# Optimization experiments

Measured on AMD Instinct MI355X. Metric: run time of the kernel, lower is better.

The kernel has to match this reference:

```python
import jax, jax.numpy as jnp
import numpy as np

B, S = 128, 72
ITER = 16
D_MODEL, D_INPUT = 1024, 512
MEM = 25
HEADS, DH = 8, 64
N_SO, N_SA = 256, 64
NUM_CLASSES = 1968
MH = 16
VOCAB, TED = 32, 128
SA_SZ = N_SA * (N_SA + 1) // 2  # 2080
SO_SZ = N_SO * (N_SO + 1) // 2  # 32896
I_A, J_A = np.triu_indices(N_SA)
I_O, J_O = np.triu_indices(N_SO)


def _ln(x, g, b):
    m = x.mean(-1, keepdims=True)
    v = ((x - m) ** 2).mean(-1, keepdims=True)
    return (x - m) / jnp.sqrt(v + 1e-5) * g + b


def _glu(x):
    a, g = jnp.split(x, 2, axis=-1)
    return a * jax.nn.sigmoid(g)


def setup_inputs():
    key = jax.random.key(0)
    ks = iter(jax.random.split(key, 32))

    def u(shape, s):
        return jax.random.uniform(next(ks), shape, jnp.float32, -s, s)

    return {
        "x": jax.random.randint(next(ks), (B, S), 0, VOCAB),
        "emb": u((VOCAB, TED), 1.0),
        "kv_w": u((TED, D_INPUT), (1.0 / TED) ** 0.5),
        "kv_b": jnp.zeros((D_INPUT,), jnp.float32),
        "kv_ln_g": jnp.ones((D_INPUT,), jnp.float32),
        "kv_ln_b": jnp.zeros((D_INPUT,), jnp.float32),
        "q_w": u((SA_SZ, D_INPUT), (1.0 / SA_SZ) ** 0.5),
        "q_b": jnp.zeros((D_INPUT,), jnp.float32),
        "in_proj_w": u((D_INPUT, 3 * D_INPUT), (1.0 / D_INPUT) ** 0.5),
        "in_proj_b": jnp.zeros((3 * D_INPUT,), jnp.float32),
        "out_proj_w": u((D_INPUT, D_INPUT), (1.0 / D_INPUT) ** 0.5),
        "out_proj_b": jnp.zeros((D_INPUT,), jnp.float32),
        "syn_w": u((D_INPUT + D_MODEL, 2 * D_MODEL), (1.0 / (D_INPUT + D_MODEL)) ** 0.5),
        "syn_b": jnp.zeros((2 * D_MODEL,), jnp.float32),
        "syn_ln_g": jnp.ones((D_MODEL,), jnp.float32),
        "syn_ln_b": jnp.zeros((D_MODEL,), jnp.float32),
        "tp1_w": u((MEM, 2 * MH, D_MODEL), 1.0 / (MEM + 2 * MH) ** 0.5),
        "tp1_b": jnp.zeros((1, D_MODEL, 2 * MH), jnp.float32),
        "tp2_w": u((MH, 2, D_MODEL), 1.0 / (MH + 2) ** 0.5),
        "tp2_b": jnp.zeros((1, D_MODEL, 2), jnp.float32),
        "start_act": u((D_MODEL,), (1.0 / D_MODEL) ** 0.5),
        "start_trace": u((D_MODEL, MEM), (1.0 / (D_MODEL + MEM)) ** 0.5),
        "decay_action": jnp.zeros((SA_SZ,), jnp.float32),
        "decay_out": jnp.zeros((SO_SZ,), jnp.float32),
        "out_w": u((SO_SZ, NUM_CLASSES), (1.0 / SO_SZ) ** 0.5),
        "out_b": jnp.zeros((NUM_CLASSES,), jnp.float32),
    }


def _forward(x, emb, kv_w, kv_b, kv_ln_g, kv_ln_b, q_w, q_b, in_proj_w, in_proj_b,
             out_proj_w, out_proj_b, syn_w, syn_b, syn_ln_g, syn_ln_b,
             tp1_w, tp1_b, tp2_w, tp2_b, start_act, start_trace,
             decay_action, decay_out, out_w, out_b):
    Bn = x.shape[0]
    # kv features: embed -> linear -> layernorm  (B,S,D_INPUT)
    kv = _ln(emb[x] @ kv_w + kv_b, kv_ln_g, kv_ln_b)
    Wq, Wk, Wv = jnp.split(in_proj_w, 3, axis=1)
    bq, bk, bv = jnp.split(in_proj_b, 3, axis=0)
    K = (kv @ Wk + bk).reshape(Bn, -1, HEADS, DH)  # (B,S,H,Dh)
    V = (kv @ Wv + bv).reshape(Bn, -1, HEADS, DH)
    # decayed running-sync coefficients (decay params clamped to [0,15])
    r_a = jnp.exp(-jnp.clip(decay_action, 0.0, 15.0))
    r_o = jnp.exp(-jnp.clip(decay_out, 0.0, 15.0))
    act0 = jnp.broadcast_to(start_act, (Bn, D_MODEL))
    trace0 = jnp.broadcast_to(start_trace, (Bn, D_MODEL, MEM))
    so0 = act0[:, :N_SO]
    a_o0 = so0[:, I_O] * so0[:, J_O]           # initial out-sync alpha
    b_o0 = jnp.ones_like(a_o0)
    a_a0 = jnp.zeros((Bn, SA_SZ), kv.dtype)    # None-init == zeros under update rule
    b_a0 = jnp.zeros((Bn, SA_SZ), kv.dtype)

    def step(carry, _):
        act, trace, a_a, b_a, a_o, b_o = carry
        # action synchronisation (last N_SA neurons, triu outer product)
        sa = act[:, -N_SA:]
        a_a = r_a * a_a + sa[:, I_A] * sa[:, J_A]
        b_a = r_a * b_a + 1.0
        sync_a = a_a / jnp.sqrt(b_a)
        # single-query multihead attention over kv
        q = sync_a @ q_w + q_b
        qh = (q @ Wq + bq).reshape(Bn, HEADS, DH)
        scores = jnp.einsum('bhd,bshd->bhs', qh, K) / (DH ** 0.5)
        attn = jax.nn.softmax(scores, axis=-1)
        o = jnp.einsum('bhs,bshd->bhd', attn, V).reshape(Bn, D_INPUT)
        o = o @ out_proj_w + out_proj_b
        # synapses: concat -> linear -> GLU -> layernorm
        pre = jnp.concatenate([o, act], axis=-1)
        state = _ln(_glu(pre @ syn_w + syn_b), syn_ln_g, syn_ln_b)
        # shift trace, append new state
        trace = jnp.concatenate([trace[:, :, 1:], state[:, :, None]], axis=-1)
        # per-neuron NLM: SuperLinear -> GLU -> SuperLinear -> GLU -> squeeze
        h = _glu(jnp.einsum('bdm,mhd->bdh', trace, tp1_w) + tp1_b)      # (B,D,MH)
        act = _glu(jnp.einsum('bdm,mhd->bdh', h, tp2_w) + tp2_b)[..., 0]  # (B,D)
        # out synchronisation (first N_SO neurons)
        so = act[:, :N_SO]
        a_o = r_o * a_o + so[:, I_O] * so[:, J_O]
        b_o = r_o * b_o + 1.0
        sync_o = a_o / jnp.sqrt(b_o)
        pred = sync_o @ out_w + out_b                                   # (B,C)
        lp = jax.nn.log_softmax(pred, axis=-1)
        ne = -jnp.sum(jnp.exp(lp) * lp, axis=-1) / jnp.log(jnp.float32(NUM_CLASSES))
        cert = jnp.stack([ne, 1.0 - ne], axis=-1)                       # (B,2)
        return (act, trace, a_a, b_a, a_o, b_o), (pred, cert)

    _, (preds, certs) = jax.lax.scan(step, (act0, trace0, a_a0, b_a0, a_o0, b_o0), None, length=ITER)
    predictions = jnp.moveaxis(preds, 0, -1)   # (B,C,ITER)
    certainties = jnp.moveaxis(certs, 0, -1)   # (B,2,ITER)
    return predictions, certainties


def reference(x, emb, kv_w, kv_b, kv_ln_g, kv_ln_b, q_w, q_b, in_proj_w, in_proj_b,
              out_proj_w, out_proj_b, syn_w, syn_b, syn_ln_g, syn_ln_b,
              tp1_w, tp1_b, tp2_w, tp2_b, start_act, start_trace,
              decay_action, decay_out, out_w, out_b):
    return _forward(x, emb, kv_w, kv_b, kv_ln_g, kv_ln_b, q_w, q_b, in_proj_w, in_proj_b,
                    out_proj_w, out_proj_b, syn_w, syn_b, syn_ln_g, syn_ln_b,
                    tp1_w, tp1_b, tp2_w, tp2_b, start_act, start_trace,
                    decay_action, decay_out, out_w, out_b)
```

## Files before the change

kernel.cpp:

```cpp
#include <hip/hip_runtime.h>
#include <math.h>

#define BB 128
#define SS 72
#define NITER 16
#define D_IN 512
#define D_MODEL 1024
#define MEMN 25
#define HEADS 8
#define DHH 64
#define N_SO 256
#define N_SA 64
#define SA_SZ 2080
#define SO_SZ 32896
#define NCLS 1968
#define TED 128
#define VOCAB 32
#define ROWS (BB*SS)
#define TRACE_SLOTS (MEMN + NITER)

#define BGN 64
#define BGKS 16
#define BGKLEN 2056
#define BGSTEPS 33
#define NPART 1984
#define WHLD 1984
#define WCHUNKS 124
#define SYNZ 6

typedef _Float16 half_t;
typedef _Float16 half8 __attribute__((ext_vector_type(8)));
typedef float f32x4v __attribute__((ext_vector_type(4)));

__device__ __forceinline__ float sigmoidf_(float x){ return 1.f/(1.f+expf(-x)); }

__device__ __forceinline__ float bsum256(float v, float* red){
  int tid = threadIdx.x; red[tid] = v; __syncthreads();
#pragma unroll
  for (int s = 128; s > 0; s >>= 1){ if (tid < s) red[tid] += red[tid+s]; __syncthreads(); }
  float r = red[0]; __syncthreads(); return r;
}

__device__ __forceinline__ long triu_off(int n, int i){
  return (long)i*n - ((long)i*(i-1))/2;
}

__device__ __forceinline__ int swzA(int b){ return b ^ (((b>>9)&1)<<5); }

__global__ void k_conv(const float* __restrict__ src, half_t* __restrict__ dst, int n){
  int gid = blockIdx.x*256 + threadIdx.x;
  if (gid < n) dst[gid] = (half_t)src[gid];
}

__global__ void k_convslice(const float* __restrict__ src, int ldsrc, int col0,
                            half_t* __restrict__ dst, int rows, int cols){
  int gid = blockIdx.x*256 + threadIdx.x;
  if (gid >= rows*cols) return;
  int r = gid / cols, c = gid % cols;
  dst[gid] = (half_t)src[(size_t)r*ldsrc + col0 + c];
}

__global__ void k_embed_h(const int* __restrict__ x, const half_t* __restrict__ embh,
                          half_t* __restrict__ out){
  int gid = blockIdx.x*256 + threadIdx.x;
  if (gid >= ROWS*(TED/8)) return;
  int row = gid >> 4, c0 = (gid & 15)*8;
  *(half8*)(out + (size_t)row*TED + c0) = *(const half8*)(embh + (size_t)x[row]*TED + c0);
}

__global__ void k_init_pairs(int n, int npairs, const float* __restrict__ decay,
                             int2* __restrict__ pairs, float* __restrict__ rv){
  int p = blockIdx.x*256 + threadIdx.x;
  if (p >= npairs) return;
  double nn = (double)n;
  double disc = (2.0*nn+1.0)*(2.0*nn+1.0) - 8.0*(double)p;
  int i = (int)floor(((2.0*nn+1.0) - sqrt(disc))*0.5);
  if (i < 0) i = 0; if (i > n-1) i = n-1;
  while (i+1 < n && triu_off(n, i+1) <= (long)p) i++;
  while (i > 0 && triu_off(n, i) > (long)p) i--;
  int j = i + (int)((long)p - triu_off(n, i));
  pairs[p] = make_int2(i, j);
  float dc = decay[p]; dc = fminf(fmaxf(dc, 0.f), 15.f);
  rv[p] = expf(-dc);
}

__global__ void k_init_act(const float* __restrict__ sa, float* __restrict__ act){
  int gid = blockIdx.x*256 + threadIdx.x;
  if (gid >= BB*D_MODEL) return;
  act[gid] = sa[gid & 1023];
}

__global__ void k_zero(float* __restrict__ p, int n){
  int gid = blockIdx.x*256 + threadIdx.x;
  if (gid < n) p[gid] = 0.f;
}

__global__ void k_init_trace(const float* __restrict__ st, float* __restrict__ trace){
  int gid = blockIdx.x*256 + threadIdx.x;
  if (gid >= BB*MEMN*D_MODEL) return;
  int d = gid & 1023;
  int m = (gid >> 10) % MEMN;
  int b = (gid >> 10) / MEMN;
  trace[(size_t)b*TRACE_SLOTS*D_MODEL + (size_t)m*D_MODEL + d] = st[d*MEMN + m];
}

__global__ void k_init_ao(const float* __restrict__ sa, const int2* __restrict__ pairs,
                          float* __restrict__ ao){
  int p = blockIdx.x*256 + threadIdx.x;
  if (p >= SO_SZ) return;
  int b = blockIdx.y;
  int2 ij = pairs[p];
  ao[(size_t)b*SO_SZ + p] = sa[ij.x]*sa[ij.y];
}

__global__ void k_convw(const float* __restrict__ W, half_t* __restrict__ Wh){
  int gid = blockIdx.x*256 + threadIdx.x;
  if (gid >= SO_SZ*WCHUNKS) return;
  int row = gid / WCHUNKS, ch = gid - row*WCHUNKS;
  int c0 = ch*16;
  half_t* dst = Wh + (size_t)row*WHLD + c0;
  if (ch < 123){
    const float4* src = (const float4*)(W + (size_t)row*NCLS + c0);
    float4 f0 = src[0], f1 = src[1], f2 = src[2], f3 = src[3];
    half8 h0, h1;
    h0[0]=(half_t)f0.x; h0[1]=(half_t)f0.y; h0[2]=(half_t)f0.z; h0[3]=(half_t)f0.w;
    h0[4]=(half_t)f1.x; h0[5]=(half_t)f1.y; h0[6]=(half_t)f1.z; h0[7]=(half_t)f1.w;
    h1[0]=(half_t)f2.x; h1[1]=(half_t)f2.y; h1[2]=(half_t)f2.z; h1[3]=(half_t)f2.w;
    h1[4]=(half_t)f3.x; h1[5]=(half_t)f3.y; h1[6]=(half_t)f3.z; h1[7]=(half_t)f3.w;
    *(half8*)dst = h0; *(half8*)(dst+8) = h1;
  } else {
    half8 zz;
#pragma unroll
    for (int j = 0; j < 8; j++) zz[j] = (half_t)0.f;
    *(half8*)dst = zz; *(half8*)(dst+8) = zz;
  }
}

__global__ void k_colsum(const float* __restrict__ vec, const float* __restrict__ W,
                         int ldw, const float* __restrict__ addb,
                         float* __restrict__ out, int N, int K){
  int col = blockIdx.x*256 + threadIdx.x;
  if (col >= N) return;
  float s = addb ? addb[col] : 0.f;
  for (int k = 0; k < K; k++) s = fmaf(vec[k], W[(size_t)k*ldw + col], s);
  out[col] = s;
}

template<int MB>
__global__ void k_gemm(const float* __restrict__ A, int lda,
                       const float* __restrict__ W, int ldw, int wrow0, int wcol0,
                       const float* __restrict__ bias,
                       float* __restrict__ C, int ldc, int N, int K){
  constexpr int KC = 32;
  const int tid = threadIdx.x;
  const int col = blockIdx.x*256 + tid;
  const int row0 = blockIdx.y*MB;
  __shared__ float As[MB][KC];
  float acc[MB];
#pragma unroll
  for (int r = 0; r < MB; r++) acc[r] = 0.f;
  for (int kk = 0; kk < K; kk += KC){
    __syncthreads();
    for (int idx = tid; idx < MB*KC; idx += 256){
      int r = idx / KC, k = idx % KC;
      As[r][k] = A[(size_t)(row0+r)*lda + kk + k];
    }
    __syncthreads();
#pragma unroll
    for (int k = 0; k < KC; k++){
      float w = W[(size_t)(wrow0+kk+k)*ldw + wcol0 + col];
#pragma unroll
      for (int r = 0; r < MB; r++) acc[r] = fmaf(As[r][k], w, acc[r]);
    }
  }
#pragma unroll
  for (int r = 0; r < MB; r++){
    size_t o = (size_t)(row0+r)*ldc + col;
    C[o] = acc[r] + (bias ? bias[col] : 0.f);
  }
}

__global__ __launch_bounds__(256)
void k_pgemm(const half_t* __restrict__ Ah, int ldah,
             const half_t* __restrict__ Wh16, const float* __restrict__ bias,
             float* __restrict__ C, int ksteps){
  __shared__ half_t As[2][128*64];
  __shared__ half_t Ws[2][64*66];
  const int tid = threadIdx.x;
  const int nb0 = blockIdx.x * 64;
  const int row0 = blockIdx.y * 128;
  const int l = tid & 63, wv = tid >> 6;
  const int mw = (wv >> 1) * 64, nw = (wv & 1) * 32;
  const int c = l & 15, g = l >> 4;

  f32x4v acc[4][2];
#pragma unroll
  for (int i = 0; i < 4; i++)
#pragma unroll
    for (int j2 = 0; j2 < 2; j2++)
#pragma unroll
      for (int r = 0; r < 4; r++) acc[i][j2][r] = 0.f;

  auto stage = [&](int s, int buf){
#pragma unroll
    for (int it = 0; it < 4; it++){
      int ch = tid + it*256;
      int m = ch >> 3, kl = (ch & 7)*8;
      half8 v = *(const half8*)(Ah + (size_t)(row0+m)*ldah + s*64 + kl);
      *(half8*)((char*)(&As[buf][0]) + swzA(ch*16)) = v;
    }
    {
      int k = tid >> 2, cs = (tid & 3) * 16;
      const half_t* wr = Wh16 + (size_t)(s*64 + k) * D_IN + nb0 + cs;
      char* dst = (char*)(&Ws[buf][0]) + (size_t)(k*66 + cs) * 2;
      union { half8 v; unsigned int u[4]; } p0, p1;
      p0.v = *(const half8*)wr; p1.v = *(const half8*)(wr + 8);
#pragma unroll
      for (int q = 0; q < 4; q++){
        ((unsigned int*)dst)[q]        = p0.u[q];
        ((unsigned int*)(dst + 16))[q] = p1.u[q];
      }
    }
  };

  stage(0, 0);
  __syncthreads();
  for (int s = 0; s < ksteps; s++){
    int buf = s & 1;
    if (s + 1 < ksteps) stage(s+1, buf^1);
#pragma unroll
    for (int h = 0; h < 2; h++){
      half8 a8[4];
#pragma unroll
      for (int mb = 0; mb < 4; mb++)
        a8[mb] = *(const half8*)((const char*)(&As[buf][0]) +
                   swzA(((mw + mb*16 + c)*64 + h*32 + g*8)*2));
#pragma unroll
      for (int nb = 0; nb < 2; nb++){
        half8 b8;
        const half_t* wp = &Ws[buf][(h*32 + g*8)*66 + nw + nb*16 + c];
#pragma unroll
        for (int j = 0; j < 8; j++) b8[j] = wp[j*66];
#pragma unroll
        for (int mb = 0; mb < 4; mb++)
          acc[mb][nb] = __builtin_amdgcn_mfma_f32_16x16x32_f16(a8[mb], b8, acc[mb][nb], 0, 0, 0);
      }
    }
    __syncthreads();
  }
#pragma unroll
  for (int mb = 0; mb < 4; mb++)
#pragma unroll
    for (int nb = 0; nb < 2; nb++){
      int m = mw + mb*16 + g*4;
      int n = nb0 + nw + nb*16 + c;
      float bv = bias[n];
#pragma unroll
      for (int r = 0; r < 4; r++)
        C[(size_t)(row0 + m + r) * D_IN + n] = acc[mb][nb][r] + bv;
    }
}

__global__ __launch_bounds__(256)
void k_syn16(const half_t* __restrict__ Ah, const half_t* __restrict__ Wh16,
             float* __restrict__ outp){
  __shared__ half_t As[2][128*64];
  __shared__ half_t Ws[2][64*66];
  const int tid = threadIdx.x;
  const int nb0 = blockIdx.x * 64;
  const int z = blockIdx.y;
  const int l = tid & 63, wv = tid >> 6;
  const int mw = (wv >> 1) * 64, nw = (wv & 1) * 32;
  const int c = l & 15, g = l >> 4;
  const int kbase = z * 256;

  f32x4v acc[4][2];
#pragma unroll
  for (int i = 0; i < 4; i++)
#pragma unroll
    for (int j2 = 0; j2 < 2; j2++)
#pragma unroll
      for (int r = 0; r < 4; r++) acc[i][j2][r] = 0.f;

  auto stage = [&](int s, int buf){
#pragma unroll
    for (int it = 0; it < 4; it++){
      int ch = tid + it*256;
      int m = ch >> 3, kl = (ch & 7)*8;
      half8 v = *(const half8*)(Ah + (size_t)m*1536 + kbase + s*64 + kl);
      *(half8*)((char*)(&As[buf][0]) + swzA(ch*16)) = v;
    }
    {
      int k = tid >> 2, cs = (tid & 3) * 16;
      const half_t* wr = Wh16 + (size_t)(kbase + s*64 + k) * 2048 + nb0 + cs;
      char* dst = (char*)(&Ws[buf][0]) + (size_t)(k*66 + cs) * 2;
      union { half8 v; unsigned int u[4]; } p0, p1;
      p0.v = *(const half8*)wr; p1.v = *(const half8*)(wr + 8);
#pragma unroll
      for (int q = 0; q < 4; q++){
        ((unsigned int*)dst)[q]        = p0.u[q];
        ((unsigned int*)(dst + 16))[q] = p1.u[q];
      }
    }
  };

  stage(0, 0);
  __syncthreads();
  for (int s = 0; s < 4; s++){
    int buf = s & 1;
    if (s + 1 < 4) stage(s+1, buf^1);
#pragma unroll
    for (int h = 0; h < 2; h++){
      half8 a8[4];
#pragma unroll
      for (int mb = 0; mb < 4; mb++)
        a8[mb] = *(const half8*)((const char*)(&As[buf][0]) +
                   swzA(((mw + mb*16 + c)*64 + h*32 + g*8)*2));
#pragma unroll
      for (int nb = 0; nb < 2; nb++){
        half8 b8;
        const half_t* wp = &Ws[buf][(h*32 + g*8)*66 + nw + nb*16 + c];
#pragma unroll
        for (int j = 0; j < 8; j++) b8[j] = wp[j*66];
#pragma unroll
        for (int mb = 0; mb < 4; mb++)
          acc[mb][nb] = __builtin_amdgcn_mfma_f32_16x16x32_f16(a8[mb], b8, acc[mb][nb], 0, 0, 0);
      }
    }
    __syncthreads();
  }
  float* pz = outp + (size_t)z * BB * 2048;
#pragma unroll
  for (int mb = 0; mb < 4; mb++)
#pragma unroll
    for (int nb = 0; nb < 2; nb++){
      int m = mw + mb*16 + g*4;
      int n = nb0 + nw + nb*16 + c;
#pragma unroll
      for (int r = 0; r < 4; r++)
        pz[(size_t)(m + r) * 2048 + n] = acc[mb][nb][r];
    }
}

__global__ void k_cat16(const float* __restrict__ obuf, const float* __restrict__ act,
                        half_t* __restrict__ Ah){
  int gid = blockIdx.x*256 + threadIdx.x;
  if (gid >= BB*192) return;
  int row = gid / 192, c = (gid - row*192)*8;
  const float* src = (c < D_IN) ? (obuf + (size_t)row*D_IN + c)
                                : (act + (size_t)row*D_MODEL + (c - D_IN));
  float4 f0 = *(const float4*)src, f1 = *(const float4*)(src + 4);
  half8 h;
  h[0]=(half_t)f0.x; h[1]=(half_t)f0.y; h[2]=(half_t)f0.z; h[3]=(half_t)f0.w;
  h[4]=(half_t)f1.x; h[5]=(half_t)f1.y; h[6]=(half_t)f1.z; h[7]=(half_t)f1.w;
  *(half8*)(Ah + (size_t)row*1536 + c) = h;
}

__global__ void k_gemmq(const float* __restrict__ A, const float* __restrict__ W,
                        float* __restrict__ qpart){
  constexpr int KC = 32;
  const int tid = threadIdx.x;
  const int col = blockIdx.x*256 + tid;
  const int row0 = blockIdx.y*4;
  const int z = blockIdx.z;
  const int kstart = z*544;
  const int kend = min(SA_SZ, kstart + 544);
  __shared__ float As[4][KC];
  float acc[4] = {0.f,0.f,0.f,0.f};
  for (int kk = kstart; kk < kend; kk += KC){
    __syncthreads();
    for (int idx = tid; idx < 4*KC; idx += 256){
      int r = idx / KC, k = idx % KC;
      As[r][k] = A[(size_t)(row0+r)*SA_SZ + kk + k];
    }
    __syncthreads();
#pragma unroll
    for (int k = 0; k < KC; k++){
      float w = W[(size_t)(kk+k)*D_IN + col];
#pragma unroll
      for (int r = 0; r < 4; r++) acc[r] = fmaf(As[r][k], w, acc[r]);
    }
  }
#pragma unroll
  for (int r = 0; r < 4; r++)
    qpart[(size_t)z*BB*D_IN + (size_t)(row0+r)*D_IN + col] = acc[r];
}

__global__ void k_gemm2srcZ(const float* __restrict__ A1, const float* __restrict__ A2,
                            const float* __restrict__ W1, const float* __restrict__ W2,
                            float* __restrict__ outp){
  constexpr int MB = 8, KC = 32;
  const int tid = threadIdx.x;
  const int col = blockIdx.x*256 + tid;
  const int row0 = blockIdx.y*MB;
  const int z = blockIdx.z;
  __shared__ float As[MB][KC];
  float acc[MB];
#pragma unroll
  for (int r = 0; r < MB; r++) acc[r] = 0.f;
  for (int kk = z*256; kk < z*256 + 256; kk += KC){
    __syncthreads();
    for (int idx = tid; idx < MB*KC; idx += 256){
      int r = idx / KC, k = idx % KC;
      int kg = kk + k;
      As[r][k] = (kg < D_IN) ? A1[(size_t)(row0+r)*D_IN + kg]
                             : A2[(size_t)(row0+r)*D_MODEL + kg - D_IN];
    }
    __syncthreads();
    const float* Wp = (kk < D_IN) ? W1 : W2;
#pragma unroll
    for (int k = 0; k < KC; k++){
      float w = Wp[(size_t)(kk+k)*2048 + col];
#pragma unroll
      for (int r = 0; r < MB; r++) acc[r] = fmaf(As[r][k], w, acc[r]);
    }
  }
#pragma unroll
  for (int r = 0; r < MB; r++)
    outp[(size_t)z*BB*2048 + (size_t)(row0+r)*2048 + col] = acc[r];
}

__global__ void k_ln_h(const float* __restrict__ X, const float* __restrict__ g,
                       const float* __restrict__ bta, half_t* __restrict__ Y, int D){
  const int row = blockIdx.x, tid = threadIdx.x;
  __shared__ float red[256];
  const float* xr = X + (size_t)row*D;
  float s = 0.f;
  for (int c = tid; c < D; c += 256) s += xr[c];
  float mean = bsum256(s, red) / (float)D;
  float s2 = 0.f;
  for (int c = tid; c < D; c += 256){ float d = xr[c]-mean; s2 += d*d; }
  float var = bsum256(s2, red) / (float)D;
  float inv = 1.f / sqrtf(var + 1e-5f);
  half_t* yr = Y + (size_t)row*D;
  for (int c = tid; c < D; c += 256) yr[c] = (half_t)((xr[c]-mean)*inv*g[c] + bta[c]);
}

__global__ void k_glu_ln(const float* __restrict__ synpart, const float* __restrict__ bias2,
                         const float* __restrict__ g, const float* __restrict__ bta,
                         float* __restrict__ traceSlot){
  const int b = blockIdx.x, tid = threadIdx.x;
  __shared__ float vals[D_MODEL];
  __shared__ float red[256];
  for (int c = tid; c < 1024; c += 256){
    float a = bias2[c], gg = bias2[c+1024];
#pragma unroll
    for (int z = 0; z < SYNZ; z++){
      const float* sp = synpart + (size_t)z*BB*2048 + (size_t)b*2048;
      a  += sp[c];
      gg += sp[c+1024];
    }
    vals[c] = a * sigmoidf_(gg);
  }
  __syncthreads();
  float s = 0.f;
  for (int c = tid; c < 1024; c += 256) s += vals[c];
  float mean = bsum256(s, red) * (1.f/1024.f);
  float s2 = 0.f;
  for (int c = tid; c < 1024; c += 256){ float d = vals[c]-mean; s2 += d*d; }
  float var = bsum256(s2, red) * (1.f/1024.f);
  float inv = 1.f / sqrtf(var + 1e-5f);
  float* out = traceSlot + (size_t)b*(TRACE_SLOTS*D_MODEL);
  for (int c = tid; c < 1024; c += 256) out[c] = (vals[c]-mean)*inv*g[c] + bta[c];
}

__global__ void k_attn(const float* __restrict__ qpart, const float* __restrict__ bqf,
                       const float* __restrict__ Km, const float* __restrict__ Vm,
                       float* __restrict__ o){
  const int bh = blockIdx.x, b = bh >> 3, h = bh & 7;
  const int tid = threadIdx.x;
  __shared__ float qs[DHH];
  __shared__ float attn[SS];
  __shared__ float red[128];
  if (tid < DHH){
    int d = h*DHH + tid;
    float qv = bqf[d];
#pragma unroll
    for (int z = 0; z < 4; z++) qv += qpart[(size_t)z*BB*D_IN + (size_t)b*D_IN + d];
    qs[tid] = qv;
  }
  __syncthreads();
  float sc = -1e30f;
  if (tid < SS){
    const float* kp = Km + ((size_t)(b*SS+tid)*HEADS + h)*DHH;
    float d = 0.f;
#pragma unroll
    for (int i = 0; i < DHH; i++) d = fmaf(qs[i], kp[i], d);
    sc = d * 0.125f;
  }
  red[tid] = sc; __syncthreads();
  for (int s2 = 64; s2 > 0; s2 >>= 1){ if (tid < s2) red[tid] = fmaxf(red[tid], red[tid+s2]); __syncthreads(); }
  float m = red[0]; __syncthreads();
  float e = (tid < SS) ? expf(sc - m) : 0.f;
  red[tid] = e; __syncthreads();
  for (int s2 = 64; s2 > 0; s2 >>= 1){ if (tid < s2) red[tid] += red[tid+s2]; __syncthreads(); }
  float inv = 1.f / red[0]; __syncthreads();
  if (tid < SS) attn[tid] = e * inv;
  __syncthreads();
  if (tid < DHH){
    const float* vp = Vm + ((size_t)(b*SS)*HEADS + h)*DHH + tid;
    float acc = 0.f;
    for (int s2 = 0; s2 < SS; s2++) acc = fmaf(attn[s2], vp[(size_t)s2*D_IN], acc);
    o[(size_t)b*D_IN + h*DHH + tid] = acc;
  }
}

__global__ void k_neuron(const float* __restrict__ trace,
                         const float* __restrict__ tp1w, const float* __restrict__ tp1b,
                         const float* __restrict__ tp2w, const float* __restrict__ tp2b,
                         float* __restrict__ act, int t){
  int gid = blockIdx.x*256 + threadIdx.x;
  if (gid >= BB*D_MODEL) return;
  int b = gid >> 10, d = gid & 1023;
  const float* tr = trace + (size_t)b*(TRACE_SLOTS*D_MODEL) + (size_t)(t+1)*D_MODEL + d;
  float trv[MEMN];
#pragma unroll
  for (int m = 0; m < MEMN; m++) trv[m] = tr[(size_t)m*D_MODEL];
  float o0 = tp2b[d*2+0], o1 = tp2b[d*2+1];
#pragma unroll
  for (int j = 0; j < 16; j++){
    const float* wpj = tp1w + (size_t)j*1024 + d;
    const float* wpg = tp1w + (size_t)(j+16)*1024 + d;
    float hj = tp1b[d*32 + j];
    float hg = tp1b[d*32 + j + 16];
#pragma unroll
    for (int m = 0; m < MEMN; m++){
      float tv = trv[m];
      hj = fmaf(tv, wpj[(size_t)m*32*1024], hj);
      hg = fmaf(tv, wpg[(size_t)m*32*1024], hg);
    }
    float hgv = hj * sigmoidf_(hg);
    o0 = fmaf(hgv, tp2w[(size_t)(j*2+0)*1024 + d], o0);
    o1 = fmaf(hgv, tp2w[(size_t)(j*2+1)*1024 + d], o1);
  }
  act[gid] = o0 * sigmoidf_(o1);
}

__global__ void k_syncA(const float* __restrict__ act, const float* __restrict__ rv,
                        const int2* __restrict__ pairs, float* __restrict__ aa,
                        float* __restrict__ syncv, int t){
  int p = blockIdx.x*256 + threadIdx.x;
  if (p >= SA_SZ) return;
  int b = blockIdx.y;
  int2 ij = pairs[p];
  const float* ab = act + (size_t)b*D_MODEL + (D_MODEL - N_SA);
  float r = rv[p];
  size_t idx = (size_t)b*SA_SZ + p;
  float a = fmaf(r, aa[idx], ab[ij.x]*ab[ij.y]);
  aa[idx] = a;
  float bb = 0.f;
  for (int i = 0; i <= t; i++) bb = fmaf(r, bb, 1.f);
  syncv[idx] = a / sqrtf(bb);
}

__global__ void k_syncO(const float* __restrict__ act, const float* __restrict__ rv,
                        const int2* __restrict__ pairs, float* __restrict__ ao,
                        half_t* __restrict__ syncv, int t){
  int p = blockIdx.x*256 + threadIdx.x;
  if (p >= SO_SZ) return;
  int b = blockIdx.y;
  int2 ij = pairs[p];
  const float* ab = act + (size_t)b*D_MODEL;
  float r = rv[p];
  size_t idx = (size_t)b*SO_SZ + p;
  float a = fmaf(r, ao[idx], ab[ij.x]*ab[ij.y]);
  ao[idx] = a;
  float bb = 1.f;
  for (int i = 0; i <= t; i++) bb = fmaf(r, bb, 1.f);
  syncv[idx] = (half_t)(a / sqrtf(bb));
}

__global__ __launch_bounds__(256)
void k_bigemm2h(const half_t* __restrict__ Ah, const half_t* __restrict__ Wh,
                float* __restrict__ part){
  __shared__ half_t As[2][128*64];
  __shared__ half_t Ws[2][64*66];
  const int tid = threadIdx.x;
  const int z = blockIdx.y;
  const int nb0 = blockIdx.x * BGN;
  const int l = tid & 63, wv = tid >> 6;
  const int mw = (wv >> 1) * 64, nw = (wv & 1) * 32;
  const int c = l & 15, g = l >> 4;
  const int k0 = z * BGKLEN;

  f32x4v acc[4][2];
#pragma unroll
  for (int i = 0; i < 4; i++)
#pragma unroll
    for (int j2 = 0; j2 < 2; j2++)
#pragma unroll
      for (int r = 0; r < 4; r++) acc[i][j2][r] = 0.f;

  auto stage = [&](int s, int buf){
    const int kv = min(64, BGKLEN - s*64);
#pragma unroll
    for (int it = 0; it < 4; it++){
      int ch = tid + it*256;
      int m = ch >> 3, kg = ch & 7, kl = kg*8;
      half8 v;
      if (kl < kv) v = *(const half8*)(Ah + (size_t)m*SO_SZ + k0 + s*64 + kl);
      else {
#pragma unroll
        for (int j = 0; j < 8; j++) v[j] = (half_t)0.f;
      }
      *(half8*)((char*)(&As[buf][0]) + swzA(ch*16)) = v;
    }
    {
      int k = tid >> 2, cs = (tid & 3) * 16;
      const half_t* wr = Wh + (size_t)(k0 + s*64 + k) * WHLD + nb0 + cs;
      char* dst = (char*)(&Ws[buf][0]) + (size_t)(k*66 + cs) * 2;
      union { half8 v; unsigned int u[4]; } p0, p1;
      if (k < kv){ p0.v = *(const half8*)wr; p1.v = *(const half8*)(wr + 8); }
      else {
#pragma unroll
        for (int j = 0; j < 8; j++){ p0.v[j] = (half_t)0.f; p1.v[j] = (half_t)0.f; }
      }
#pragma unroll
      for (int q = 0; q < 4; q++){
        ((unsigned int*)dst)[q]        = p0.u[q];
        ((unsigned int*)(dst + 16))[q] = p1.u[q];
      }
    }
  };

  stage(0, 0);
  __syncthreads();
  for (int s = 0; s < BGSTEPS; s++){
    int buf = s & 1;
    if (s + 1 < BGSTEPS) stage(s+1, buf^1);
#pragma unroll
    for (int h = 0; h < 2; h++){
      half8 a8[4];
#pragma unroll
      for (int mb = 0; mb < 4; mb++)
        a8[mb] = *(const half8*)((const char*)(&As[buf][0]) +
                   swzA(((mw + mb*16 + c)*64 + h*32 + g*8)*2));
#pragma unroll
      for (int nb = 0; nb < 2; nb++){
        half8 b8;
        const half_t* wp = &Ws[buf][(h*32 + g*8)*66 + nw + nb*16 + c];
#pragma unroll
        for (int j = 0; j < 8; j++) b8[j] = wp[j*66];
#pragma unroll
        for (int mb = 0; mb < 4; mb++)
          acc[mb][nb] = __builtin_amdgcn_mfma_f32_16x16x32_f16(a8[mb], b8, acc[mb][nb], 0, 0, 0);
      }
    }
    __syncthreads();
  }
  float* pz = part + (size_t)z * 128 * NPART;
#pragma unroll
  for (int mb = 0; mb < 4; mb++)
#pragma unroll
    for (int nb = 0; nb < 2; nb++){
      int m = mw + mb*16 + g*4;
      int n = nb0 + nw + nb*16 + c;
#pragma unroll
      for (int r = 0; r < 4; r++)
        pz[(size_t)(m + r) * NPART + n] = acc[mb][nb][r];
    }
}

__global__ void k_output(const float* __restrict__ part, const float* __restrict__ outb,
                         float* __restrict__ dout, int t){
  const int b = blockIdx.x, tid = threadIdx.x;
  __shared__ float pred[NCLS];
  __shared__ float red[256];
  float lmax = -1e30f;
  for (int c = tid; c < NCLS; c += 256){
    float s = outb[c];
    const float* pp = part + (size_t)b*NPART + c;
#pragma unroll
    for (int z = 0; z < BGKS; z++) s += pp[(size_t)z*128*NPART];
    pred[c] = s;
    dout[((size_t)b*NCLS + c)*NITER + t] = s;
    lmax = fmaxf(lmax, s);
  }
  red[tid] = lmax; __syncthreads();
  for (int s2 = 128; s2 > 0; s2 >>= 1){ if (tid < s2) red[tid] = fmaxf(red[tid], red[tid+s2]); __syncthreads(); }
  float m = red[0]; __syncthreads();
  float se = 0.f;
  for (int c = tid; c < NCLS; c += 256) se += expf(pred[c]-m);
  float Z = bsum256(se, red);
  float logZ = m + logf(Z);
  float ent = 0.f;
  for (int c = tid; c < NCLS; c += 256){ float lp = pred[c]-logZ; ent += expf(lp)*lp; }
  float E = bsum256(ent, red);
  if (tid == 0){
    float ne = -E * (1.f/logf((float)NCLS));
    float* cp = dout + (size_t)BB*NCLS*NITER + (size_t)b*2*NITER + t;
    cp[0]     = ne;
    cp[NITER] = 1.f - ne;
  }
}

extern "C" void kernel_launch(void* const* d_in, const int* in_sizes, int n_in,
                              void* d_out, int out_size, void* d_ws, size_t ws_size,
                              hipStream_t stream){
  const int*   x           = (const int*)  d_in[0];
  const float* emb         = (const float*)d_in[1];
  const float* kv_w        = (const float*)d_in[2];
  const float* kv_b        = (const float*)d_in[3];
  const float* kv_ln_g     = (const float*)d_in[4];
  const float* kv_ln_b     = (const float*)d_in[5];
  const float* q_w         = (const float*)d_in[6];
  const float* q_b         = (const float*)d_in[7];
  const float* in_proj_w   = (const float*)d_in[8];
  const float* in_proj_b   = (const float*)d_in[9];
  const float* out_proj_w  = (const float*)d_in[10];
  const float* out_proj_b  = (const float*)d_in[11];
  const float* syn_w       = (const float*)d_in[12];
  const float* syn_b       = (const float*)d_in[13];
  const float* syn_ln_g    = (const float*)d_in[14];
  const float* syn_ln_b    = (const float*)d_in[15];
  const float* tp1_w       = (const float*)d_in[16];
  const float* tp1_b       = (const float*)d_in[17];
  const float* tp2_w       = (const float*)d_in[18];
  const float* tp2_b       = (const float*)d_in[19];
  const float* start_act   = (const float*)d_in[20];
  const float* start_trace = (const float*)d_in[21];
  const float* decay_action= (const float*)d_in[22];
  const float* decay_out   = (const float*)d_in[23];
  const float* out_w       = (const float*)d_in[24];
  const float* out_b       = (const float*)d_in[25];
  float* dout = (float*)d_out;

  float* w = (float*)d_ws;
  size_t off = 0;
  auto alloc = [&](size_t n){ n = (n + 3) & ~(size_t)3; float* p = w + off; off += n; return p; };
  float* region0 = alloc((size_t)BGKS*128*NPART);
  float* region1 = alloc((size_t)ROWS*D_IN);
  float* Kmat    = alloc((size_t)ROWS*D_IN);
  float* Vmat    = alloc((size_t)ROWS*D_IN);
  float* trace   = alloc((size_t)BB*TRACE_SLOTS*D_MODEL);
  half_t* sync_oh= (half_t*)alloc((size_t)BB*SO_SZ/2);
  float* a_a     = alloc((size_t)BB*SA_SZ);
  float* sync_a  = alloc((size_t)BB*SA_SZ);
  float* act     = alloc((size_t)BB*D_MODEL);
  float* qpart   = alloc((size_t)4*BB*D_IN);
  float* obuf    = alloc((size_t)BB*D_IN);
  float* qfw     = alloc((size_t)SA_SZ*D_IN);
  float* Wf2     = alloc((size_t)D_IN*2048);
  float* bqf     = alloc(D_IN);
  float* bias2   = alloc(2048);
  float* r_a     = alloc(SA_SZ);
  float* r_o     = alloc(SO_SZ);
  int2*  pairsA  = (int2*)alloc(2*SA_SZ);
  int2*  pairsO  = (int2*)alloc(2*SO_SZ);
  half_t* embh   = (half_t*)alloc((size_t)VOCAB*TED/2);
  half_t* kvwh   = (half_t*)alloc((size_t)TED*D_IN/2);
  half_t* Wkh    = (half_t*)alloc((size_t)D_IN*D_IN/2);
  half_t* Wvh    = (half_t*)alloc((size_t)D_IN*D_IN/2);
  half_t* Wh     = (half_t*)alloc(((size_t)SO_SZ*WHLD)/2);
  half_t* Ah16   = (half_t*)alloc((size_t)BB*1536/2);
  half_t* Wsynh  = (half_t*)alloc((size_t)1536*2048/2);
  const bool use_syn16 = (off * sizeof(float) <= ws_size);

  half_t* embx_h = (half_t*)region0;
  half_t* kvh    = (half_t*)region0;
  float* part    = region0;
  float* synpart = region0;
  float* kvbuf = region1;
  float* a_o   = region1;

  dim3 blk(256);

  k_conv<<<(VOCAB*TED+255)/256, blk, 0, stream>>>(emb, embh, VOCAB*TED);
  k_convslice<<<(TED*D_IN+255)/256, blk, 0, stream>>>(kv_w, D_IN, 0, kvwh, TED, D_IN);
  k_convslice<<<(D_IN*D_IN+255)/256, blk, 0, stream>>>(in_proj_w, 1536, 512,  Wkh, D_IN, D_IN);
  k_convslice<<<(D_IN*D_IN+255)/256, blk, 0, stream>>>(in_proj_w, 1536, 1024, Wvh, D_IN, D_IN);
  k_embed_h<<<(ROWS*(TED/8)+255)/256, blk, 0, stream>>>(x, embh, embx_h);
  k_pgemm<<<dim3(8, ROWS/128), blk, 0, stream>>>(embx_h, TED, kvwh, kv_b, kvbuf, TED/64);
  k_ln_h<<<ROWS, blk, 0, stream>>>(kvbuf, kv_ln_g, kv_ln_b, kvh, D_IN);
  k_pgemm<<<dim3(8, ROWS/128), blk, 0, stream>>>(kvh, D_IN, Wkh, in_proj_b+512,  Kmat, D_IN/64);
  k_pgemm<<<dim3(8, ROWS/128), blk, 0, stream>>>(kvh, D_IN, Wvh, in_proj_b+1024, Vmat, D_IN/64);
  k_gemm<4><<<dim3(2, SA_SZ/4), blk, 0, stream>>>(q_w, D_IN, in_proj_w, 1536, 0, 0, nullptr, qfw, D_IN, D_IN, D_IN);
  k_gemm<4><<<dim3(8, D_IN/4), blk, 0, stream>>>(out_proj_w, D_IN, syn_w, 2048, 0, 0, nullptr, Wf2, 2048, 2048, D_IN);
  k_colsum<<<2, blk, 0, stream>>>(q_b, in_proj_w, 1536, in_proj_b, bqf, D_IN, D_IN);
  k_colsum<<<8, blk, 0, stream>>>(out_proj_b, syn_w, 2048, syn_b, bias2, 2048, D_IN);
  k_convw<<<(SO_SZ*WCHUNKS+255)/256, blk, 0, stream>>>(out_w, Wh);
  if (use_syn16){
    k_conv<<<(512*2048+255)/256, blk, 0, stream>>>(Wf2, Wsynh, 512*2048);
    k_conv<<<(1024*2048+255)/256, blk, 0, stream>>>(syn_w + (size_t)512*2048, Wsynh + (size_t)512*2048, 1024*2048);
  }
  k_init_pairs<<<(SA_SZ+255)/256, blk, 0, stream>>>(N_SA, SA_SZ, decay_action, pairsA, r_a);
  k_init_pairs<<<(SO_SZ+255)/256, blk, 0, stream>>>(N_SO, SO_SZ, decay_out,    pairsO, r_o);
  k_init_act<<<(BB*D_MODEL+255)/256, blk, 0, stream>>>(start_act, act);
  k_zero<<<(BB*SA_SZ+255)/256, blk, 0, stream>>>(a_a, BB*SA_SZ);
  k_init_trace<<<(BB*MEMN*D_MODEL+255)/256, blk, 0, stream>>>(start_trace, trace);
  k_init_ao<<<dim3((SO_SZ+255)/256, BB), blk, 0, stream>>>(start_act, pairsO, a_o);

  for (int t = 0; t < NITER; t++){
    k_syncA<<<dim3((SA_SZ+255)/256, BB), blk, 0, stream>>>(act, r_a, pairsA, a_a, sync_a, t);
    k_gemmq<<<dim3(2, 32, 4), blk, 0, stream>>>(sync_a, qfw, qpart);
    k_attn<<<BB*HEADS, 128, 0, stream>>>(qpart, bqf, Kmat, Vmat, obuf);
    if (use_syn16){
      k_cat16<<<(BB*192+255)/256, blk, 0, stream>>>(obuf, act, Ah16);
      k_syn16<<<dim3(32, SYNZ), blk, 0, stream>>>(Ah16, Wsynh, synpart);
    } else {
      k_gemm2srcZ<<<dim3(8, 16, SYNZ), blk, 0, stream>>>(obuf, act, Wf2, syn_w, synpart);
    }
    k_glu_ln<<<BB, blk, 0, stream>>>(synpart, bias2, syn_ln_g, syn_ln_b, trace + (size_t)(MEMN+t)*D_MODEL);
    k_neuron<<<(BB*D_MODEL+255)/256, blk, 0, stream>>>(trace, tp1_w, tp1_b, tp2_w, tp2_b, act, t);
    k_syncO<<<dim3((SO_SZ+255)/256, BB), blk, 0, stream>>>(act, r_o, pairsO, a_o, sync_oh, t);
    k_bigemm2h<<<dim3(31, BGKS), blk, 0, stream>>>(sync_oh, Wh, part);
    k_output<<<BB, blk, 0, stream>>>(part, out_b, dout, t);
  }
}
```

Baseline: 3.041 ms.

## Fuse syncA into gemmq, drop cat16, store q weights in half, merge setup conversions

The action-synchronisation update is computed inside the q GEMM's A-tile load, using ping-pong buffers for the decay state so the separate syncA kernel and the sync_a buffer go away. The fp16 concat input for the synapse GEMM is written directly by k_attn, k_neuron and k_init_act, which removes k_cat16. The fused q weight matrix is converted to fp16 to halve its reads. Several setup conversion kernels are merged into fewer launches. Each gemmq block now recomputes the sync values, including the per-element decay loop, and the half-precision q weights add rounding error.

```diff
diff --git a/kernel.cpp b/kernel.cpp
--- a/kernel.cpp
+++ b/kernel.cpp
@@ -52,12 +52,28 @@
   if (gid < n) dst[gid] = (half_t)src[gid];
 }
 
-__global__ void k_convslice(const float* __restrict__ src, int ldsrc, int col0,
-                            half_t* __restrict__ dst, int rows, int cols){
+#define CV0 (VOCAB*TED)
+#define CV1 (CV0 + TED*D_IN)
+#define CV2 (CV1 + D_IN*D_IN)
+#define CV3 (CV2 + D_IN*D_IN)
+__global__ void k_convall(const float* __restrict__ emb, const float* __restrict__ kv_w,
+                          const float* __restrict__ in_proj_w,
+                          half_t* __restrict__ embh, half_t* __restrict__ kvwh,
+                          half_t* __restrict__ Wkh, half_t* __restrict__ Wvh){
   int gid = blockIdx.x*256 + threadIdx.x;
-  if (gid >= rows*cols) return;
-  int r = gid / cols, c = gid % cols;
-  dst[gid] = (half_t)src[(size_t)r*ldsrc + col0 + c];
+  if (gid < CV0){ embh[gid] = (half_t)emb[gid]; return; }
+  if (gid < CV1){ int i = gid - CV0; kvwh[i] = (half_t)kv_w[i]; return; }
+  if (gid < CV2){ int i = gid - CV1; int r = i >> 9, c = i & 511;
+                  Wkh[i] = (half_t)in_proj_w[(size_t)r*1536 + 512 + c]; return; }
+  if (gid < CV3){ int i = gid - CV2; int r = i >> 9, c = i & 511;
+                  Wvh[i] = (half_t)in_proj_w[(size_t)r*1536 + 1024 + c]; return; }
+}
+
+__global__ void k_convsyn(const float* __restrict__ Wf2, const float* __restrict__ syn_w,
+                          half_t* __restrict__ Wsynh){
+  int gid = blockIdx.x*256 + threadIdx.x;
+  if (gid >= 1536*2048) return;
+  Wsynh[gid] = (half_t)((gid < 512*2048) ? Wf2[gid] : syn_w[gid]);
 }
 
 __global__ void k_embed_h(const int* __restrict__ x, const half_t* __restrict__ embh,
@@ -84,10 +100,14 @@
   rv[p] = expf(-dc);
 }
 
-__global__ void k_init_act(const float* __restrict__ sa, float* __restrict__ act){
+__global__ void k_init_act(const float* __restrict__ sa, float* __restrict__ act,
+                           half_t* __restrict__ Ah16){
   int gid = blockIdx.x*256 + threadIdx.x;
   if (gid >= BB*D_MODEL) return;
-  act[gid] = sa[gid & 1023];
+  int b = gid >> 10, d = gid & 1023;
+  float v = sa[d];
+  act[gid] = v;
+  Ah16[(size_t)b*1536 + 512 + d] = (half_t)v;
 }
 
 __global__ void k_zero(float* __restrict__ p, int n){
@@ -342,22 +362,10 @@
     }
 }
 
-__global__ void k_cat16(const float* __restrict__ obuf, const float* __restrict__ act,
-                        half_t* __restrict__ Ah){
-  int gid = blockIdx.x*256 + threadIdx.x;
-  if (gid >= BB*192) return;
-  int row = gid / 192, c = (gid - row*192)*8;
-  const float* src = (c < D_IN) ? (obuf + (size_t)row*D_IN + c)
-                                : (act + (size_t)row*D_MODEL + (c - D_IN));
-  float4 f0 = *(const float4*)src, f1 = *(const float4*)(src + 4);
-  half8 h;
-  h[0]=(half_t)f0.x; h[1]=(half_t)f0.y; h[2]=(half_t)f0.z; h[3]=(half_t)f0.w;
-  h[4]=(half_t)f1.x; h[5]=(half_t)f1.y; h[6]=(half_t)f1.z; h[7]=(half_t)f1.w;
-  *(half8*)(Ah + (size_t)row*1536 + c) = h;
-}
-
-__global__ void k_gemmq(const float* __restrict__ A, const float* __restrict__ W,
-                        float* __restrict__ qpart){
+__global__ void k_gemmq(const float* __restrict__ act,
+                        const float* __restrict__ r_a, const int2* __restrict__ pairsA,
+                        const float* __restrict__ aaIn, float* __restrict__ aaOut,
+                        const half_t* __restrict__ Wh, float* __restrict__ qpart, int t){
   constexpr int KC = 32;
   const int tid = threadIdx.x;
   const int col = blockIdx.x*256 + tid;
@@ -365,18 +373,29 @@
   const int z = blockIdx.z;
   const int kstart = z*544;
   const int kend = min(SA_SZ, kstart + 544);
+  const bool writer = (blockIdx.x == 0);
   __shared__ float As[4][KC];
   float acc[4] = {0.f,0.f,0.f,0.f};
   for (int kk = kstart; kk < kend; kk += KC){
     __syncthreads();
-    for (int idx = tid; idx < 4*KC; idx += 256){
-      int r = idx / KC, k = idx % KC;
-      As[r][k] = A[(size_t)(row0+r)*SA_SZ + kk + k];
+    if (tid < 4*KC){
+      int r = tid >> 5, k = tid & 31;
+      int p = kk + k;
+      int b = row0 + r;
+      int2 ij = pairsA[p];
+      const float* ab = act + (size_t)b*D_MODEL + (D_MODEL - N_SA);
+      float rv = r_a[p];
+      size_t idx = (size_t)b*SA_SZ + p;
+      float a = fmaf(rv, aaIn[idx], ab[ij.x]*ab[ij.y]);
+      if (writer) aaOut[idx] = a;
+      float bb = 0.f;
+      for (int i = 0; i <= t; i++) bb = fmaf(rv, bb, 1.f);
+      As[r][k] = a / sqrtf(bb);
     }
     __syncthreads();
 #pragma unroll
     for (int k = 0; k < KC; k++){
-      float w = W[(size_t)(kk+k)*D_IN + col];
+      float w = (float)Wh[(size_t)(kk+k)*D_IN + col];
 #pragma unroll
       for (int r = 0; r < 4; r++) acc[r] = fmaf(As[r][k], w, acc[r]);
     }
@@ -466,7 +485,7 @@
 
 __global__ void k_attn(const float* __restrict__ qpart, const float* __restrict__ bqf,
                        const float* __restrict__ Km, const float* __restrict__ Vm,
-                       float* __restrict__ o){
+                       float* __restrict__ o, half_t* __restrict__ Ah16){
   const int bh = blockIdx.x, b = bh >> 3, h = bh & 7;
   const int tid = threadIdx.x;
   __shared__ float qs[DHH];
@@ -501,14 +520,16 @@
     const float* vp = Vm + ((size_t)(b*SS)*HEADS + h)*DHH + tid;
     float acc = 0.f;
     for (int s2 = 0; s2 < SS; s2++) acc = fmaf(attn[s2], vp[(size_t)s2*D_IN], acc);
-    o[(size_t)b*D_IN + h*DHH + tid] = acc;
+    int d = h*DHH + tid;
+    o[(size_t)b*D_IN + d] = acc;
+    Ah16[(size_t)b*1536 + d] = (half_t)acc;
   }
 }
 
 __global__ void k_neuron(const float* __restrict__ trace,
                          const float* __restrict__ tp1w, const float* __restrict__ tp1b,
                          const float* __restrict__ tp2w, const float* __restrict__ tp2b,
-                         float* __restrict__ act, int t){
+                         float* __restrict__ act, half_t* __restrict__ Ah16, int t){
   int gid = blockIdx.x*256 + threadIdx.x;
   if (gid >= BB*D_MODEL) return;
   int b = gid >> 10, d = gid & 1023;
@@ -533,24 +554,9 @@
     o0 = fmaf(hgv, tp2w[(size_t)(j*2+0)*1024 + d], o0);
     o1 = fmaf(hgv, tp2w[(size_t)(j*2+1)*1024 + d], o1);
   }
-  act[gid] = o0 * sigmoidf_(o1);
-}
-
-__global__ void k_syncA(const float* __restrict__ act, const float* __restrict__ rv,
-                        const int2* __restrict__ pairs, float* __restrict__ aa,
-                        float* __restrict__ syncv, int t){
-  int p = blockIdx.x*256 + threadIdx.x;
-  if (p >= SA_SZ) return;
-  int b = blockIdx.y;
-  int2 ij = pairs[p];
-  const float* ab = act + (size_t)b*D_MODEL + (D_MODEL - N_SA);
-  float r = rv[p];
-  size_t idx = (size_t)b*SA_SZ + p;
-  float a = fmaf(r, aa[idx], ab[ij.x]*ab[ij.y]);
-  aa[idx] = a;
-  float bb = 0.f;
-  for (int i = 0; i <= t; i++) bb = fmaf(r, bb, 1.f);
-  syncv[idx] = a / sqrtf(bb);
+  float v = o0 * sigmoidf_(o1);
+  act[gid] = v;
+  Ah16[(size_t)b*1536 + 512 + d] = (half_t)v;
 }
 
 __global__ void k_syncO(const float* __restrict__ act, const float* __restrict__ rv,
@@ -734,8 +740,7 @@
   float* Vmat    = alloc((size_t)ROWS*D_IN);
   float* trace   = alloc((size_t)BB*TRACE_SLOTS*D_MODEL);
   half_t* sync_oh= (half_t*)alloc((size_t)BB*SO_SZ/2);
-  float* a_a     = alloc((size_t)BB*SA_SZ);
-  float* sync_a  = alloc((size_t)BB*SA_SZ);
+  float* a_aP    = alloc((size_t)2*BB*SA_SZ);
   float* act     = alloc((size_t)BB*D_MODEL);
   float* qpart   = alloc((size_t)4*BB*D_IN);
   float* obuf    = alloc((size_t)BB*D_IN);
@@ -751,6 +756,7 @@
   half_t* kvwh   = (half_t*)alloc((size_t)TED*D_IN/2);
   half_t* Wkh    = (half_t*)alloc((size_t)D_IN*D_IN/2);
   half_t* Wvh    = (half_t*)alloc((size_t)D_IN*D_IN/2);
+  half_t* qfwh   = (half_t*)alloc((size_t)SA_SZ*D_IN/2);
   half_t* Wh     = (half_t*)alloc(((size_t)SO_SZ*WHLD)/2);
   half_t* Ah16   = (half_t*)alloc((size_t)BB*1536/2);
   half_t* Wsynh  = (half_t*)alloc((size_t)1536*2048/2);
@@ -765,10 +771,7 @@
 
   dim3 blk(256);
 
-  k_conv<<<(VOCAB*TED+255)/256, blk, 0, stream>>>(emb, embh, VOCAB*TED);
-  k_convslice<<<(TED*D_IN+255)/256, blk, 0, stream>>>(kv_w, D_IN, 0, kvwh, TED, D_IN);
-  k_convslice<<<(D_IN*D_IN+255)/256, blk, 0, stream>>>(in_proj_w, 1536, 512,  Wkh, D_IN, D_IN);
-  k_convslice<<<(D_IN*D_IN+255)/256, blk, 0, stream>>>(in_proj_w, 1536, 1024, Wvh, D_IN, D_IN);
+  k_convall<<<(CV3+255)/256, blk, 0, stream>>>(emb, kv_w, in_proj_w, embh, kvwh, Wkh, Wvh);
   k_embed_h<<<(ROWS*(TED/8)+255)/256, blk, 0, stream>>>(x, embh, embx_h);
   k_pgemm<<<dim3(8, ROWS/128), blk, 0, stream>>>(embx_h, TED, kvwh, kv_b, kvbuf, TED/64);
   k_ln_h<<<ROWS, blk, 0, stream>>>(kvbuf, kv_ln_g, kv_ln_b, kvh, D_IN);
@@ -776,32 +779,30 @@
   k_pgemm<<<dim3(8, ROWS/128), blk, 0, stream>>>(kvh, D_IN, Wvh, in_proj_b+1024, Vmat, D_IN/64);
   k_gemm<4><<<dim3(2, SA_SZ/4), blk, 0, stream>>>(q_w, D_IN, in_proj_w, 1536, 0, 0, nullptr, qfw, D_IN, D_IN, D_IN);
   k_gemm<4><<<dim3(8, D_IN/4), blk, 0, stream>>>(out_proj_w, D_IN, syn_w, 2048, 0, 0, nullptr, Wf2, 2048, 2048, D_IN);
+  k_conv<<<(SA_SZ*D_IN+255)/256, blk, 0, stream>>>(qfw, qfwh, SA_SZ*D_IN);
   k_colsum<<<2, blk, 0, stream>>>(q_b, in_proj_w, 1536, in_proj_b, bqf, D_IN, D_IN);
   k_colsum<<<8, blk, 0, stream>>>(out_proj_b, syn_w, 2048, syn_b, bias2, 2048, D_IN);
   k_convw<<<(SO_SZ*WCHUNKS+255)/256, blk, 0, stream>>>(out_w, Wh);
-  if (use_syn16){
-    k_conv<<<(512*2048+255)/256, blk, 0, stream>>>(Wf2, Wsynh, 512*2048);
-    k_conv<<<(1024*2048+255)/256, blk, 0, stream>>>(syn_w + (size_t)512*2048, Wsynh + (size_t)512*2048, 1024*2048);
-  }
+  if (use_syn16)
+    k_convsyn<<<(1536*2048+255)/256, blk, 0, stream>>>(Wf2, syn_w, Wsynh);
   k_init_pairs<<<(SA_SZ+255)/256, blk, 0, stream>>>(N_SA, SA_SZ, decay_action, pairsA, r_a);
   k_init_pairs<<<(SO_SZ+255)/256, blk, 0, stream>>>(N_SO, SO_SZ, decay_out,    pairsO, r_o);
-  k_init_act<<<(BB*D_MODEL+255)/256, blk, 0, stream>>>(start_act, act);
-  k_zero<<<(BB*SA_SZ+255)/256, blk, 0, stream>>>(a_a, BB*SA_SZ);
+  k_init_act<<<(BB*D_MODEL+255)/256, blk, 0, stream>>>(start_act, act, Ah16);
+  k_zero<<<(2*BB*SA_SZ+255)/256, blk, 0, stream>>>(a_aP, 2*BB*SA_SZ);
   k_init_trace<<<(BB*MEMN*D_MODEL+255)/256, blk, 0, stream>>>(start_trace, trace);
   k_init_ao<<<dim3((SO_SZ+255)/256, BB), blk, 0, stream>>>(start_act, pairsO, a_o);
 
   for (int t = 0; t < NITER; t++){
-    k_syncA<<<dim3((SA_SZ+255)/256, BB), blk, 0, stream>>>(act, r_a, pairsA, a_a, sync_a, t);
-    k_gemmq<<<dim3(2, 32, 4), blk, 0, stream>>>(sync_a, qfw, qpart);
-    k_attn<<<BB*HEADS, 128, 0, stream>>>(qpart, bqf, Kmat, Vmat, obuf);
-    if (use_syn16){
-      k_cat16<<<(BB*192+255)/256, blk, 0, stream>>>(obuf, act, Ah16);
+    float* aaIn  = a_aP + (size_t)(t & 1)*BB*SA_SZ;
+    float* aaOut = a_aP + (size_t)((t+1) & 1)*BB*SA_SZ;
+    k_gemmq<<<dim3(2, 32, 4), blk, 0, stream>>>(act, r_a, pairsA, aaIn, aaOut, qfwh, qpart, t);
+    k_attn<<<BB*HEADS, 128, 0, stream>>>(qpart, bqf, Kmat, Vmat, obuf, Ah16);
+    if (use_syn16)
       k_syn16<<<dim3(32, SYNZ), blk, 0, stream>>>(Ah16, Wsynh, synpart);
-    } else {
+    else
       k_gemm2srcZ<<<dim3(8, 16, SYNZ), blk, 0, stream>>>(obuf, act, Wf2, syn_w, synpart);
-    }
     k_glu_ln<<<BB, blk, 0, stream>>>(synpart, bias2, syn_ln_g, syn_ln_b, trace + (size_t)(MEMN+t)*D_MODEL);
-    k_neuron<<<(BB*D_MODEL+255)/256, blk, 0, stream>>>(trace, tp1_w, tp1_b, tp2_w, tp2_b, act, t);
+    k_neuron<<<(BB*D_MODEL+255)/256, blk, 0, stream>>>(trace, tp1_w, tp1_b, tp2_w, tp2_b, act, Ah16, t);
     k_syncO<<<dim3((SO_SZ+255)/256, BB), blk, 0, stream>>>(act, r_o, pairsO, a_o, sync_oh, t);
     k_bigemm2h<<<dim3(31, BGKS), blk, 0, stream>>>(sync_oh, Wh, part);
     k_output<<<BB, blk, 0, stream>>>(part, out_b, dout, t);
```

Result: no change. 2.993 ms (-1.6%).
